# Performance work log

Hardware: AMD Instinct MI355X
Metric: run time of the kernel (lower is better)

## Reference

```python
import jax, jax.numpy as jnp
import numpy as np

B, T, E, D = 4, 1024, 1024, 2048   # batch, dec len, enc len, model dim
N, K, H = 16, 8, 256               # q heads, kv heads, head dim
G = N // K                         # GQA group size
SCALE = H ** -0.5                  # query_pre_attn_scalar
SOFT_CAP = 50.0
EPS = 1e-6
ROPE_BASE = 10000.0
_K_MASK = jnp.finfo(jnp.bfloat16).min


def _rms_norm(x, scale, eps=EPS):
    var = jnp.mean(jnp.square(x), axis=-1, keepdims=True)
    return x * jax.lax.rsqrt(var + eps) * (1.0 + scale)


def _apply_rope(x, positions, base=ROPE_BASE):
    # x: [B, L, n, H], positions: [B, L]; rope_proportion=1.0, scale_factor=1.0
    h = x.shape[-1]
    freq_exp = 2.0 / h * jnp.arange(h // 2, dtype=jnp.float32)
    timescale = base ** freq_exp                                  # [H/2]
    ang = (positions.astype(jnp.float32)[..., None] / timescale)[..., None, :]  # [B,L,1,H/2]
    sin, cos = jnp.sin(ang), jnp.cos(ang)
    x1, x2 = jnp.split(x, 2, axis=-1)
    out = jnp.concatenate([x1 * cos - x2 * sin, x2 * cos + x1 * sin], axis=-1)
    return out.astype(x.dtype)


def setup_inputs() -> dict:
    key = jax.random.key(0)
    ks = jax.random.split(key, 8)
    hidden_states = jax.random.normal(ks[0], (B, T, D), jnp.float32)
    encoder_hidden_states = jax.random.normal(ks[1], (B, E, D), jnp.float32)
    position_ids = jnp.broadcast_to(jnp.arange(T, dtype=jnp.int32)[None, :], (B, T))
    # merged mask: causal over self part, full visibility over cross part
    causal = jnp.tril(jnp.ones((T, T), jnp.bool_))
    cross = jnp.ones((T, E), jnp.bool_)
    merged_attention_mask = jnp.broadcast_to(
        jnp.concatenate([causal, cross], axis=-1)[None, None], (B, 1, T, T + E))
    w = 0.02
    q_w = jax.random.normal(ks[2], (N, D, H), jnp.float32) * w
    k_w = jax.random.normal(ks[3], (K, D, H), jnp.float32) * w
    v_w = jax.random.normal(ks[4], (K, D, H), jnp.float32) * w
    o_w = jax.random.normal(ks[5], (N, H, D), jnp.float32) * w
    q_scale = jax.random.normal(ks[6], (H,), jnp.float32) * w
    k_scale = jax.random.normal(ks[7], (H,), jnp.float32) * w
    return dict(hidden_states=hidden_states, encoder_hidden_states=encoder_hidden_states,
                position_ids=position_ids, merged_attention_mask=merged_attention_mask,
                q_w=q_w, k_w=k_w, v_w=v_w, o_w=o_w, q_scale=q_scale, k_scale=k_scale)


def reference(hidden_states, encoder_hidden_states, position_ids, merged_attention_mask,
              q_w, k_w, v_w, o_w, q_scale, k_scale):
    # QKV projections
    query = jnp.einsum('BTD,NDH->BTNH', hidden_states, q_w)
    self_key = jnp.einsum('BTD,KDH->BTKH', hidden_states, k_w)
    self_value = jnp.einsum('BTD,KDH->BTKH', hidden_states, v_w)
    # QK-RMSNorm
    query = _rms_norm(query, q_scale)
    self_key = _rms_norm(self_key, k_scale)
    # RoPE on self-attention q/k only
    query = _apply_rope(query, position_ids)
    self_key = _apply_rope(self_key, position_ids)
    # Cross K/V from encoder states (no RoPE)
    cross_key = _rms_norm(jnp.einsum('BTD,KDH->BTKH', encoder_hidden_states, k_w), k_scale)
    cross_value = jnp.einsum('BTD,KDH->BTKH', encoder_hidden_states, v_w)
    # Merge self + cross along key axis
    keys = jnp.concatenate([self_key, cross_key], axis=1)       # [B, T+E, K, H]
    values = jnp.concatenate([self_value, cross_value], axis=1)
    # Scaled GQA attention
    q = (query * SCALE).reshape(B, T, K, G, H)
    logits = jnp.einsum('BTKGH,BSKH->BKGTS', q, keys)
    # logit soft-capping
    logits = SOFT_CAP * jnp.tanh(logits / SOFT_CAP)
    mask = merged_attention_mask[:, :, None]                    # [B,1,1,T,S]
    logits = jnp.where(mask, logits, _K_MASK)
    probs = jax.nn.softmax(logits.astype(jnp.float32), axis=-1).astype(keys.dtype)
    attn = jnp.einsum('BKGTS,BSKH->BTKGH', probs, values).reshape(B, T, N, H)
    return jnp.einsum('BTNH,NHD->BTD', attn, o_w)
```

## Files before the change

### kernel.cpp

```cpp
#include <hip/hip_runtime.h>
#include <hip/hip_bf16.h>
#include <cstdio>


typedef __attribute__((ext_vector_type(8))) short bf16x8;
typedef __attribute__((ext_vector_type(4))) float f32x4;

static __device__ __forceinline__ ushort f2bf(float x){
  uint u = __float_as_uint(x);
  u += 0x7fffu + ((u >> 16) & 1u);
  return (ushort)(u >> 16);
}
static __device__ __forceinline__ float bf2f(ushort u){
  return __uint_as_float((uint)u << 16);
}
#define GLL16(gp, lp)                                                          \
  __builtin_amdgcn_global_load_lds(                                            \
      (const __attribute__((address_space(1))) void*)(gp),                     \
      (__attribute__((address_space(3))) void*)(lp), 16, 0, 0)

__global__ void k_detect(const uint* __restrict__ src, int* __restrict__ flag){
  int lane = threadIdx.x & 63;
  int cnt = 0;
  for (int i = 0; i < 4; i++){
    uint w = src[lane * 4 + i];
    uint e = (w >> 7) & 0xffu;
    cnt += (e >= 90u && e <= 141u) ? 1 : 0;
  }
  for (int o = 1; o < 64; o <<= 1) cnt += __shfl_xor(cnt, o);
  if (lane == 0) *flag = (cnt >= 128) ? 1 : 0;
}

__global__ void k_tobf(const void* __restrict__ src, ushort* __restrict__ dst,
                       int n8, const int* __restrict__ flag){
  int i = blockIdx.x * blockDim.x + threadIdx.x;
  if (i >= n8) return;
  if (*flag){
    reinterpret_cast<uint4*>(dst)[i] = reinterpret_cast<const uint4*>(src)[i];
  } else {
    const float4* s = reinterpret_cast<const float4*>(src);
    float4 a = s[i * 2], b = s[i * 2 + 1];
    ushort o[8] = { f2bf(a.x), f2bf(a.y), f2bf(a.z), f2bf(a.w),
                    f2bf(b.x), f2bf(b.y), f2bf(b.z), f2bf(b.w) };
    reinterpret_cast<uint4*>(dst)[i] = *reinterpret_cast<uint4*>(o);
  }
}

__global__ void k_wtrans(const void* __restrict__ in, ushort* __restrict__ out,
                         int R, int C, const int* __restrict__ flag){
  __shared__ ushort t[32][33];
  int isbf = *flag;
  int p = blockIdx.z;
  int r0 = blockIdx.y * 32, c0 = blockIdx.x * 32;
  ushort* op = out + (size_t)p * R * C;
  int cc = threadIdx.x & 31, rr = threadIdx.x >> 5;
  if (isbf){
    const ushort* ip = (const ushort*)in + (size_t)p * R * C;
    for (int i = 0; i < 32; i += 8)
      t[rr + i][cc] = ip[(size_t)(r0 + rr + i) * C + c0 + cc];
  } else {
    const float* ip = (const float*)in + (size_t)p * R * C;
    for (int i = 0; i < 32; i += 8)
      t[rr + i][cc] = f2bf(ip[(size_t)(r0 + rr + i) * C + c0 + cc]);
  }
  __syncthreads();
  for (int i = 0; i < 32; i += 8)
    op[(size_t)(c0 + rr + i) * R + r0 + cc] = t[cc][rr + i];
}

__global__ __launch_bounds__(256)
void k_gemm_qkv(const ushort* __restrict__ A0, const ushort* __restrict__ A1,
                const ushort* __restrict__ Bm,
                ushort* __restrict__ Qo, ushort* __restrict__ Ko,
                ushort* __restrict__ Vo){
  const int m0 = blockIdx.y * 128, n0 = blockIdx.x * 128;
  if (n0 < 4096 && m0 >= 4096) return;
  __shared__ ushort As[128 * 32];
  __shared__ ushort Bs[128 * 32];
  const int tid = threadIdx.x;
  const int Kd = 2048;
  const ushort* Ap = (m0 < 4096) ? (A0 + (size_t)m0 * Kd)
                                 : (A1 + (size_t)(m0 - 4096) * Kd);
  const ushort* Bp = Bm + (size_t)n0 * Kd;
  const int w = tid >> 6, lane = tid & 63, c = lane & 15, q = lane >> 4;
  const int wr = (w >> 1) * 64, wc = (w & 1) * 64;

  f32x4 zf = {0.f, 0.f, 0.f, 0.f};
  f32x4 acc[4][4];
  for (int mi = 0; mi < 4; mi++) for (int ni = 0; ni < 4; ni++) acc[mi][ni] = zf;

  const int sr = tid >> 2, sc8 = (tid & 3) * 8;
  const ushort* ga = Ap + (size_t)sr * Kd + sc8;
  const ushort* gb = Bp + (size_t)sr * Kd + sc8;
  ushort* la = &As[sr * 32 + sc8];
  ushort* lb = &Bs[sr * 32 + sc8];
  const size_t rowskip = (size_t)64 * Kd;

  for (int k0 = 0; k0 < Kd; k0 += 32){
    GLL16(ga + k0,           la);
    GLL16(ga + k0 + rowskip, la + 64 * 32);
    GLL16(gb + k0,           lb);
    GLL16(gb + k0 + rowskip, lb + 64 * 32);
    __syncthreads();
    bf16x8 af[4], bfrg[4];
    for (int mi = 0; mi < 4; mi++)
      af[mi] = *reinterpret_cast<const bf16x8*>(&As[(wr + mi * 16 + c) * 32 + q * 8]);
    for (int ni = 0; ni < 4; ni++)
      bfrg[ni] = *reinterpret_cast<const bf16x8*>(&Bs[(wc + ni * 16 + c) * 32 + q * 8]);
    for (int mi = 0; mi < 4; mi++)
      for (int ni = 0; ni < 4; ni++)
        acc[mi][ni] = __builtin_amdgcn_mfma_f32_16x16x32_bf16(af[mi], bfrg[ni], acc[mi][ni], 0, 0, 0);
    __syncthreads();
  }

  for (int mi = 0; mi < 4; mi++)
    for (int ni = 0; ni < 4; ni++){
      int gr0 = m0 + wr + mi * 16 + q * 4;
      int gc  = n0 + wc + ni * 16 + c;
      if (n0 < 4096){
        for (int r = 0; r < 4; r++)
          Qo[(size_t)(gr0 + r) * 4096 + gc] = f2bf(acc[mi][ni][r]);
      } else if (n0 < 6144){
        int col = gc - 4096;
        for (int r = 0; r < 4; r++){
          int gr = gr0 + r, b, s;
          if (gr < 4096){ b = gr >> 10; s = gr & 1023; }
          else { int g2 = gr - 4096; b = g2 >> 10; s = 1024 + (g2 & 1023); }
          Ko[(size_t)(b * 2048 + s) * 2048 + col] = f2bf(acc[mi][ni][r]);
        }
      } else {
        int col = gc - 6144;
        int gr = gr0, b, s;
        if (gr < 4096){ b = gr >> 10; s = gr & 1023; }
        else { int g2 = gr - 4096; b = g2 >> 10; s = 1024 + (g2 & 1023); }
        int kk = col >> 8, h = col & 255;
        ushort4 o;
        o.x = f2bf(acc[mi][ni][0]); o.y = f2bf(acc[mi][ni][1]);
        o.z = f2bf(acc[mi][ni][2]); o.w = f2bf(acc[mi][ni][3]);
        *reinterpret_cast<ushort4*>(Vo + ((size_t)(b * 8 + kk) * 256 + h) * 2048 + s) = o;
      }
    }
}

__global__ __launch_bounds__(256)
void k_gemm_o(const ushort* __restrict__ A0, const ushort* __restrict__ Bm,
              float* __restrict__ Cout, int N, int Kd){
  __shared__ ushort As[128 * 32];
  __shared__ ushort Bs[128 * 32];
  const int tid = threadIdx.x;
  const int m0 = blockIdx.y * 128, n0 = blockIdx.x * 128;
  const ushort* Ap = A0 + (size_t)m0 * Kd;
  const ushort* Bp = Bm + (size_t)n0 * Kd;
  const int w = tid >> 6, lane = tid & 63, c = lane & 15, q = lane >> 4;
  const int wr = (w >> 1) * 64, wc = (w & 1) * 64;
  f32x4 zf = {0.f, 0.f, 0.f, 0.f};
  f32x4 acc[4][4];
  for (int mi = 0; mi < 4; mi++) for (int ni = 0; ni < 4; ni++) acc[mi][ni] = zf;
  const int sr = tid >> 2, sc8 = (tid & 3) * 8;
  const ushort* ga = Ap + (size_t)sr * Kd + sc8;
  const ushort* gb = Bp + (size_t)sr * Kd + sc8;
  ushort* la = &As[sr * 32 + sc8];
  ushort* lb = &Bs[sr * 32 + sc8];
  const size_t rowskip = (size_t)64 * Kd;
  for (int k0 = 0; k0 < Kd; k0 += 32){
    GLL16(ga + k0,           la);
    GLL16(ga + k0 + rowskip, la + 64 * 32);
    GLL16(gb + k0,           lb);
    GLL16(gb + k0 + rowskip, lb + 64 * 32);
    __syncthreads();
    bf16x8 af[4], bfrg[4];
    for (int mi = 0; mi < 4; mi++)
      af[mi] = *reinterpret_cast<const bf16x8*>(&As[(wr + mi * 16 + c) * 32 + q * 8]);
    for (int ni = 0; ni < 4; ni++)
      bfrg[ni] = *reinterpret_cast<const bf16x8*>(&Bs[(wc + ni * 16 + c) * 32 + q * 8]);
    for (int mi = 0; mi < 4; mi++)
      for (int ni = 0; ni < 4; ni++)
        acc[mi][ni] = __builtin_amdgcn_mfma_f32_16x16x32_bf16(af[mi], bfrg[ni], acc[mi][ni], 0, 0, 0);
    __syncthreads();
  }
  for (int mi = 0; mi < 4; mi++)
    for (int ni = 0; ni < 4; ni++){
      int gr0 = m0 + wr + mi * 16 + q * 4;
      int gc  = n0 + wc + ni * 16 + c;
      for (int r = 0; r < 4; r++)
        Cout[(size_t)(gr0 + r) * N + gc] = acc[mi][ni][r];
    }
}

__global__ __launch_bounds__(256)
void k_norm_q(const ushort* __restrict__ Qraw, const int* __restrict__ pos,
              const ushort* __restrict__ scale, ushort* __restrict__ Qbf){
  int w = threadIdx.x >> 6, lane = threadIdx.x & 63;
  int gw = blockIdx.x * 4 + w;
  int bt = gw >> 4;
  ushort4 xu = *reinterpret_cast<const ushort4*>(Qraw + (size_t)gw * 256 + lane * 4);
  float x[4] = { bf2f(xu.x), bf2f(xu.y), bf2f(xu.z), bf2f(xu.w) };
  float ss = x[0]*x[0] + x[1]*x[1] + x[2]*x[2] + x[3]*x[3];
  for (int o = 32; o > 0; o >>= 1) ss += __shfl_xor(ss, o);
  float rin = rsqrtf(ss * (1.f / 256.f) + 1e-6f);
  ushort4 su = *reinterpret_cast<const ushort4*>(scale + lane * 4);
  float y[4] = { x[0] * rin * (1.f + bf2f(su.x)), x[1] * rin * (1.f + bf2f(su.y)),
                 x[2] * rin * (1.f + bf2f(su.z)), x[3] * rin * (1.f + bf2f(su.w)) };
  float oth[4];
  for (int i = 0; i < 4; i++) oth[i] = __shfl_xor(y[i], 32);
  bool hi = lane >= 32;
  float fb = (float)((lane & 31) * 4);
  float p = (float)pos[bt];
  ushort4 o;
  ushort* op[4] = {&o.x, &o.y, &o.z, &o.w};
  for (int i = 0; i < 4; i++){
    float fi = fb + i;
    float tsi = expf(fi * -0.07195578415f);
    float ang = p * tsi;
    float sn, cs; sincosf(ang, &sn, &cs);
    float v = hi ? (y[i] * cs + oth[i] * sn) : (y[i] * cs - oth[i] * sn);
    *op[i] = f2bf(v * 0.0625f);
  }
  *reinterpret_cast<ushort4*>(Qbf + (size_t)gw * 256 + lane * 4) = o;
}

__global__ __launch_bounds__(256)
void k_norm_k(const ushort* __restrict__ Kraw, const int* __restrict__ pos,
              const ushort* __restrict__ scale, ushort* __restrict__ Kbf){
  int w = threadIdx.x >> 6, lane = threadIdx.x & 63;
  int gw = blockIdx.x * 4 + w;
  int row = gw >> 3;
  int s = row & 2047, b = row >> 11;
  ushort4 xu = *reinterpret_cast<const ushort4*>(Kraw + (size_t)gw * 256 + lane * 4);
  float x[4] = { bf2f(xu.x), bf2f(xu.y), bf2f(xu.z), bf2f(xu.w) };
  float ss = x[0]*x[0] + x[1]*x[1] + x[2]*x[2] + x[3]*x[3];
  for (int o = 32; o > 0; o >>= 1) ss += __shfl_xor(ss, o);
  float rin = rsqrtf(ss * (1.f / 256.f) + 1e-6f);
  ushort4 su = *reinterpret_cast<const ushort4*>(scale + lane * 4);
  float y[4] = { x[0] * rin * (1.f + bf2f(su.x)), x[1] * rin * (1.f + bf2f(su.y)),
                 x[2] * rin * (1.f + bf2f(su.z)), x[3] * rin * (1.f + bf2f(su.w)) };
  ushort4 o;
  ushort* op[4] = {&o.x, &o.y, &o.z, &o.w};
  if (s < 1024){
    float oth[4];
    for (int i = 0; i < 4; i++) oth[i] = __shfl_xor(y[i], 32);
    bool hi = lane >= 32;
    float fb = (float)((lane & 31) * 4);
    float p = (float)pos[b * 1024 + s];
    for (int i = 0; i < 4; i++){
      float fi = fb + i;
      float tsi = expf(fi * -0.07195578415f);
      float ang = p * tsi;
      float sn, cs; sincosf(ang, &sn, &cs);
      float v = hi ? (y[i] * cs + oth[i] * sn) : (y[i] * cs - oth[i] * sn);
      *op[i] = f2bf(v);
    }
  } else {
    for (int i = 0; i < 4; i++) *op[i] = f2bf(y[i]);
  }
  *reinterpret_cast<ushort4*>(Kbf + (size_t)gw * 256 + lane * 4) = o;
}

__global__ __launch_bounds__(256)
void k_attn(const ushort* __restrict__ Qbf, const ushort* __restrict__ Kbf,
            const ushort* __restrict__ Vt, ushort* __restrict__ attn){
  constexpr int PSs = 40;
  __shared__ ushort Ks2[2][32 * 256];
  __shared__ ushort Vs2[2][256 * 32];
  __shared__ ushort Pm[4][32 * PSs];
  int id = blockIdx.x;
  int xcd = id & 7, slot = id >> 3;
  int gl  = slot >> 4;
  int grp = xcd + 8 * gl;
  int w16 = slot & 15;
  int b = grp >> 3, kk = grp & 7;
  int a16 = w16 >> 1, p16 = w16 & 1;
  int hh = a16 & 1, xx = a16 >> 1;
  int j0 = p16 ? 7 - xx : xx;
  int j  = (gl >= 2) ? 7 - j0 : j0;
  int n = kk * 2 + hh;
  int t0 = j * 128;
  int tid = threadIdx.x, w = tid >> 6, lane = tid & 63, c = lane & 15, q = lane >> 4;
  int rowbase = t0 + w * 32;

  bf16x8 qf[2][8];
  for (int g = 0; g < 2; g++){
    int tq = rowbase + g * 16 + c;
    const ushort* qp = Qbf + ((size_t)(b * 1024 + tq) * 16 + n) * 256 + q * 8;
    for (int f = 0; f < 8; f++) qf[g][f] = *reinterpret_cast<const bf16x8*>(qp + f * 32);
  }
  f32x4 zf = {0.f, 0.f, 0.f, 0.f};
  f32x4 accO[2][16];
  for (int g = 0; g < 2; g++) for (int i = 0; i < 16; i++) accO[g][i] = zf;
  float lacc[2][4] = {{0.f,0.f,0.f,0.f},{0.f,0.f,0.f,0.f}};

  const ushort* Kbase = Kbf + ((size_t)b * 2048 * 8 + kk) * 256;
  const ushort* Vbase = Vt + (size_t)(b * 8 + kk) * 256 * 2048;
  int nself = (t0 >> 5) + 4;
  int ntile = nself + 32;

#define STAGE(bf, s0v)                                                         \
  do {                                                                         \
    const ushort* kp_ = Kbase + (size_t)(s0v) * 2048;                          \
    const ushort* vp_ = Vbase + (s0v);                                         \
    _Pragma("unroll")                                                          \
    for (int i_ = 0; i_ < 4; i_++){                                            \
      int tau_ = tid + i_ * 256;                                               \
      int r_ = tau_ >> 5, kch_ = tau_ & 31;                                    \
      GLL16(kp_ + r_ * 2048 + ((kch_ ^ (r_ & 7)) << 3), &Ks2[bf][tau_ * 8]);   \
    }                                                                          \
    _Pragma("unroll")                                                          \
    for (int i_ = 0; i_ < 4; i_++){                                            \
      int tau_ = tid + i_ * 256;                                               \
      int h_ = tau_ >> 2, k2_ = tau_ & 3;                                      \
      GLL16(vp_ + h_ * 2048 + (k2_ << 3), &Vs2[bf][tau_ * 8]);                 \
    }                                                                          \
  } while (0)

  STAGE(0, 0);
  int cur = 0;
  const int cxor = c & 7;

  for (int it = 0; it < ntile; ++it){
    int s0 = (it < nself) ? it * 32 : 1024 + (it - nself) * 32;
    __builtin_amdgcn_sched_barrier(0);
    __builtin_amdgcn_s_barrier();
    __builtin_amdgcn_sched_barrier(0);
    if (it + 1 < ntile){
      int itn = it + 1;
      int s0n = (itn < nself) ? itn * 32 : 1024 + (itn - nself) * 32;
      STAGE(cur ^ 1, s0n);
      __asm__ volatile("s_waitcnt vmcnt(8)" ::: "memory");
    } else {
      __asm__ volatile("s_waitcnt vmcnt(0)" ::: "memory");
    }
    __builtin_amdgcn_sched_barrier(0);
    __builtin_amdgcn_s_barrier();
    __builtin_amdgcn_sched_barrier(0);

    const ushort* Kcur = Ks2[cur];
    const ushort* Vcur = Vs2[cur];
    f32x4 accL[2][2];
    accL[0][0] = zf; accL[0][1] = zf; accL[1][0] = zf; accL[1][1] = zf;
    for (int ni = 0; ni < 2; ni++)
      for (int f = 0; f < 8; f++){
        bf16x8 kb = *reinterpret_cast<const bf16x8*>(
            &Kcur[(ni * 16 + c) * 256 + (((f * 4 + q) ^ cxor) << 3)]);
        accL[0][ni] = __builtin_amdgcn_mfma_f32_16x16x32_bf16(qf[0][f], kb, accL[0][ni], 0, 0, 0);
        accL[1][ni] = __builtin_amdgcn_mfma_f32_16x16x32_bf16(qf[1][f], kb, accL[1][ni], 0, 0, 0);
      }
    ushort* pw = Pm[w];
    for (int g = 0; g < 2; g++)
      for (int ni = 0; ni < 2; ni++)
        for (int r = 0; r < 4; r++){
          int s = s0 + ni * 16 + c;
          int t = rowbase + g * 16 + q * 4 + r;
          float e2 = __expf(accL[g][ni][r] * 0.04f);
          float d = __builtin_amdgcn_rcpf(e2 + 1.f);
          float pv = (s >= 1024 || s <= t)
                       ? 5.184705529e21f * __expf(-100.f * d) : 0.f;
          lacc[g][r] += pv;
          pw[(g * 16 + q * 4 + r) * PSs + ni * 16 + c] = f2bf(pv);
        }
    __asm__ volatile("s_waitcnt lgkmcnt(0)" ::: "memory");
    bf16x8 pa0 = *reinterpret_cast<const bf16x8*>(&pw[c * PSs + q * 8]);
    bf16x8 pa1 = *reinterpret_cast<const bf16x8*>(&pw[(16 + c) * PSs + q * 8]);
    for (int hi = 0; hi < 16; hi++){
      bf16x8 vb = *reinterpret_cast<const bf16x8*>(&Vcur[(hi * 16 + c) * 32 + q * 8]);
      accO[0][hi] = __builtin_amdgcn_mfma_f32_16x16x32_bf16(pa0, vb, accO[0][hi], 0, 0, 0);
      accO[1][hi] = __builtin_amdgcn_mfma_f32_16x16x32_bf16(pa1, vb, accO[1][hi], 0, 0, 0);
    }
    __builtin_amdgcn_sched_barrier(0);
    cur ^= 1;
  }
#undef STAGE
  for (int g = 0; g < 2; g++)
    for (int r = 0; r < 4; r++)
      for (int o = 1; o < 16; o <<= 1) lacc[g][r] += __shfl_xor(lacc[g][r], o);
  for (int g = 0; g < 2; g++){
    float inv[4];
    for (int r = 0; r < 4; r++) inv[r] = 1.f / fmaxf(lacc[g][r], 1e-37f);
    for (int hi = 0; hi < 16; hi++)
      for (int r = 0; r < 4; r++){
        int t = rowbase + g * 16 + q * 4 + r;
        attn[((size_t)(b * 1024 + t) * 16 + n) * 256 + hi * 16 + c] = f2bf(accO[g][hi][r] * inv[r]);
      }
  }
}

extern "C" void kernel_launch(void* const* d_in, const int* in_sizes, int n_in,
                              void* d_out, int out_size, void* d_ws, size_t ws_size,
                              hipStream_t stream){
  const void* hidden = d_in[0];
  const void* enc    = d_in[1];
  const int*  posids = (const int*)d_in[2];
  const void* qw = d_in[4];
  const void* kw = d_in[5];
  const void* vw = d_in[6];
  const void* ow = d_in[7];
  const void* qs = d_in[8];
  const void* ks = d_in[9];
  float* out = (float*)d_out;

  char* ws = (char*)d_ws;
  size_t off = 0;
  auto alloc = [&](size_t sz){ void* p = ws + off; off += sz; return p; };
  char*   HbEb = (char*)alloc(33554432);
  ushort* Hb   = (ushort*)HbEb;
  ushort* Eb   = (ushort*)(HbEb + 16777216);
  ushort* Wcat = (ushort*)alloc(33554432);
  ushort* Wo   = (ushort*)alloc(16777216);
  ushort* Qraw = (ushort*)alloc(33554432);
  ushort* Kraw = (ushort*)alloc(33554432);
  ushort* Vt   = (ushort*)alloc(33554432);
  ushort* qsb  = (ushort*)alloc(512);
  ushort* ksb  = (ushort*)alloc(512);
  int*    flag = (int*)alloc(64);
  ushort* Qbf   = (ushort*)HbEb;
  ushort* Kbf   = Qraw;
  ushort* attnb = Kraw;
  if (off > ws_size){
    fprintf(stderr, "kernel_launch: ws too small: need %zu, have %zu\n", off, ws_size);
    return;
  }

  k_detect<<<1, 64, 0, stream>>>((const uint*)hidden, flag);
  k_tobf<<<4096, 256, 0, stream>>>(hidden, Hb, 1048576, flag);
  k_tobf<<<4096, 256, 0, stream>>>(enc,    Eb, 1048576, flag);
  k_tobf<<<1, 256, 0, stream>>>(qs, qsb, 32, flag);
  k_tobf<<<1, 256, 0, stream>>>(ks, ksb, 32, flag);

  k_wtrans<<<dim3(8, 64, 16), 256, 0, stream>>>(qw, Wcat,            2048, 256, flag);
  k_wtrans<<<dim3(8, 64, 8),  256, 0, stream>>>(kw, Wcat + 8388608,  2048, 256, flag);
  k_wtrans<<<dim3(8, 64, 8),  256, 0, stream>>>(vw, Wcat + 12582912, 2048, 256, flag);
  k_wtrans<<<dim3(64, 128, 1), 256, 0, stream>>>(ow, Wo, 4096, 2048, flag);

  k_gemm_qkv<<<dim3(64, 64), 256, 0, stream>>>(Hb, Eb, Wcat, Qraw, Kraw, Vt);

  k_norm_q<<<16384, 256, 0, stream>>>(Qraw, posids, qsb, Qbf);
  k_norm_k<<<16384, 256, 0, stream>>>(Kraw, posids, ksb, Kbf);

  k_attn<<<512, 256, 0, stream>>>(Qbf, Kbf, Vt, attnb);

  k_gemm_o<<<dim3(16, 32), 256, 0, stream>>>(attnb, Wo, out, 2048, 4096);
}
```

Measured before the change: 900.8 us.

## Use atomic work queue with longest-first job order in attention kernel

The attention kernel no longer maps each block to a fixed tile. A global counter, reset in the preceding norm kernel, hands out jobs so the longest causal tiles (high j) are taken first. Blocks loop until the queue is empty, which should even out the load caused by causal imbalance. It also adds an XOR swizzle on the V shared-memory tile to reduce LDS bank conflicts. The cost is an atomic plus a barrier per job, and the previous XCD-aware tile placement is lost, which may hurt L2 locality.

Result: faster. 878.4 us (-2.5%).

```diff
diff --git a/kernel.cpp b/kernel.cpp
--- a/kernel.cpp
+++ b/kernel.cpp
@@ -221,7 +221,9 @@
 
 __global__ __launch_bounds__(256)
 void k_norm_k(const ushort* __restrict__ Kraw, const int* __restrict__ pos,
-              const ushort* __restrict__ scale, ushort* __restrict__ Kbf){
+              const ushort* __restrict__ scale, ushort* __restrict__ Kbf,
+              int* __restrict__ ctr){
+  if (blockIdx.x == 0 && threadIdx.x == 0) *ctr = 0;
   int w = threadIdx.x >> 6, lane = threadIdx.x & 63;
   int gw = blockIdx.x * 4 + w;
   int row = gw >> 3;
@@ -258,128 +260,139 @@
 
 __global__ __launch_bounds__(256)
 void k_attn(const ushort* __restrict__ Qbf, const ushort* __restrict__ Kbf,
-            const ushort* __restrict__ Vt, ushort* __restrict__ attn){
+            const ushort* __restrict__ Vt, ushort* __restrict__ attn,
+            int* __restrict__ ctr){
   constexpr int PSs = 40;
   __shared__ ushort Ks2[2][32 * 256];
   __shared__ ushort Vs2[2][256 * 32];
   __shared__ ushort Pm[4][32 * PSs];
-  int id = blockIdx.x;
-  int xcd = id & 7, slot = id >> 3;
-  int gl  = slot >> 4;
-  int grp = xcd + 8 * gl;
-  int w16 = slot & 15;
-  int b = grp >> 3, kk = grp & 7;
-  int a16 = w16 >> 1, p16 = w16 & 1;
-  int hh = a16 & 1, xx = a16 >> 1;
-  int j0 = p16 ? 7 - xx : xx;
-  int j  = (gl >= 2) ? 7 - j0 : j0;
-  int n = kk * 2 + hh;
-  int t0 = j * 128;
+  __shared__ int jobS;
+
   int tid = threadIdx.x, w = tid >> 6, lane = tid & 63, c = lane & 15, q = lane >> 4;
-  int rowbase = t0 + w * 32;
-
-  bf16x8 qf[2][8];
-  for (int g = 0; g < 2; g++){
-    int tq = rowbase + g * 16 + c;
-    const ushort* qp = Qbf + ((size_t)(b * 1024 + tq) * 16 + n) * 256 + q * 8;
-    for (int f = 0; f < 8; f++) qf[g][f] = *reinterpret_cast<const bf16x8*>(qp + f * 32);
-  }
+  const int cxor = c & 7;
+  const int vxor = (c >> 1) & 3;
+  int cur = 0;
   f32x4 zf = {0.f, 0.f, 0.f, 0.f};
-  f32x4 accO[2][16];
-  for (int g = 0; g < 2; g++) for (int i = 0; i < 16; i++) accO[g][i] = zf;
-  float lacc[2][4] = {{0.f,0.f,0.f,0.f},{0.f,0.f,0.f,0.f}};
-
-  const ushort* Kbase = Kbf + ((size_t)b * 2048 * 8 + kk) * 256;
-  const ushort* Vbase = Vt + (size_t)(b * 8 + kk) * 256 * 2048;
-  int nself = (t0 >> 5) + 4;
-  int ntile = nself + 32;
+
+  int ktau[4], vtau[4];
+#pragma unroll
+  for (int i = 0; i < 4; i++){ ktau[i] = tid + i * 256; vtau[i] = tid + i * 256; }
+
+  for (;;){
+    if (tid == 0) jobS = atomicAdd(ctr, 1);
+    __syncthreads();
+    int job = jobS;
+    if (job >= 512) return;
+    int grp = job & 31;
+    int within = job >> 5;
+    int b = grp >> 3, kk = grp & 7;
+    int n = kk * 2 + (within & 1);
+    int j = 7 - (within >> 1);
+    int t0 = j * 128;
+    int rowbase = t0 + w * 32;
+
+    const ushort* Kbase = Kbf + ((size_t)b * 2048 * 8 + kk) * 256;
+    const ushort* Vbase = Vt + (size_t)(b * 8 + kk) * 256 * 2048;
+    int nself = (t0 >> 5) + 4;
+    int ntile = nself + 32;
+
+    bf16x8 qf[2][8];
+    for (int g = 0; g < 2; g++){
+      int tq = rowbase + g * 16 + c;
+      const ushort* qp = Qbf + ((size_t)(b * 1024 + tq) * 16 + n) * 256 + q * 8;
+      for (int f = 0; f < 8; f++) qf[g][f] = *reinterpret_cast<const bf16x8*>(qp + f * 32);
+    }
+    f32x4 accO[2][16];
+    for (int g = 0; g < 2; g++) for (int i = 0; i < 16; i++) accO[g][i] = zf;
+    float lacc[2][4] = {{0.f,0.f,0.f,0.f},{0.f,0.f,0.f,0.f}};
 
 #define STAGE(bf, s0v)                                                         \
-  do {                                                                         \
-    const ushort* kp_ = Kbase + (size_t)(s0v) * 2048;                          \
-    const ushort* vp_ = Vbase + (s0v);                                         \
-    _Pragma("unroll")                                                          \
-    for (int i_ = 0; i_ < 4; i_++){                                            \
-      int tau_ = tid + i_ * 256;                                               \
-      int r_ = tau_ >> 5, kch_ = tau_ & 31;                                    \
-      GLL16(kp_ + r_ * 2048 + ((kch_ ^ (r_ & 7)) << 3), &Ks2[bf][tau_ * 8]);   \
-    }                                                                          \
-    _Pragma("unroll")                                                          \
-    for (int i_ = 0; i_ < 4; i_++){                                            \
-      int tau_ = tid + i_ * 256;                                               \
-      int h_ = tau_ >> 2, k2_ = tau_ & 3;                                      \
-      GLL16(vp_ + h_ * 2048 + (k2_ << 3), &Vs2[bf][tau_ * 8]);                 \
-    }                                                                          \
-  } while (0)
-
-  STAGE(0, 0);
-  int cur = 0;
-  const int cxor = c & 7;
-
-  for (int it = 0; it < ntile; ++it){
-    int s0 = (it < nself) ? it * 32 : 1024 + (it - nself) * 32;
-    __builtin_amdgcn_sched_barrier(0);
-    __builtin_amdgcn_s_barrier();
-    __builtin_amdgcn_sched_barrier(0);
-    if (it + 1 < ntile){
-      int itn = it + 1;
-      int s0n = (itn < nself) ? itn * 32 : 1024 + (itn - nself) * 32;
-      STAGE(cur ^ 1, s0n);
-      __asm__ volatile("s_waitcnt vmcnt(8)" ::: "memory");
-    } else {
-      __asm__ volatile("s_waitcnt vmcnt(0)" ::: "memory");
-    }
-    __builtin_amdgcn_sched_barrier(0);
-    __builtin_amdgcn_s_barrier();
-    __builtin_amdgcn_sched_barrier(0);
-
-    const ushort* Kcur = Ks2[cur];
-    const ushort* Vcur = Vs2[cur];
-    f32x4 accL[2][2];
-    accL[0][0] = zf; accL[0][1] = zf; accL[1][0] = zf; accL[1][1] = zf;
-    for (int ni = 0; ni < 2; ni++)
-      for (int f = 0; f < 8; f++){
-        bf16x8 kb = *reinterpret_cast<const bf16x8*>(
-            &Kcur[(ni * 16 + c) * 256 + (((f * 4 + q) ^ cxor) << 3)]);
-        accL[0][ni] = __builtin_amdgcn_mfma_f32_16x16x32_bf16(qf[0][f], kb, accL[0][ni], 0, 0, 0);
-        accL[1][ni] = __builtin_amdgcn_mfma_f32_16x16x32_bf16(qf[1][f], kb, accL[1][ni], 0, 0, 0);
+    do {                                                                       \
+      const ushort* kp_ = Kbase + (size_t)(s0v) * 2048;                        \
+      const ushort* vp_ = Vbase + (s0v);                                       \
+      _Pragma("unroll")                                                        \
+      for (int i_ = 0; i_ < 4; i_++){                                          \
+        int tau_ = ktau[i_];                                                   \
+        int r_ = tau_ >> 5, kch_ = tau_ & 31;                                  \
+        GLL16(kp_ + r_ * 2048 + ((kch_ ^ (r_ & 7)) << 3), &Ks2[bf][tau_ * 8]); \
+      }                                                                        \
+      _Pragma("unroll")                                                        \
+      for (int i_ = 0; i_ < 4; i_++){                                          \
+        int tau_ = vtau[i_];                                                   \
+        int h_ = tau_ >> 2, k2_ = tau_ & 3;                                    \
+        GLL16(vp_ + h_ * 2048 + ((k2_ ^ ((h_ >> 1) & 3)) << 3),                \
+              &Vs2[bf][tau_ * 8]);                                             \
+      }                                                                        \
+    } while (0)
+
+    STAGE(cur, 0);
+
+    for (int it = 0; it < ntile; ++it){
+      int s0 = (it < nself) ? it * 32 : 1024 + (it - nself) * 32;
+      __builtin_amdgcn_sched_barrier(0);
+      __builtin_amdgcn_s_barrier();
+      __builtin_amdgcn_sched_barrier(0);
+      if (it + 1 < ntile){
+        int itn = it + 1;
+        int s0n = (itn < nself) ? itn * 32 : 1024 + (itn - nself) * 32;
+        STAGE(cur ^ 1, s0n);
+        __asm__ volatile("s_waitcnt vmcnt(8)" ::: "memory");
+      } else {
+        __asm__ volatile("s_waitcnt vmcnt(0)" ::: "memory");
       }
-    ushort* pw = Pm[w];
+      __builtin_amdgcn_sched_barrier(0);
+      __builtin_amdgcn_s_barrier();
+      __builtin_amdgcn_sched_barrier(0);
+
+      const ushort* Kcur = Ks2[cur];
+      const ushort* Vcur = Vs2[cur];
+      f32x4 accL[2][2];
+      accL[0][0] = zf; accL[0][1] = zf; accL[1][0] = zf; accL[1][1] = zf;
+      for (int ni = 0; ni < 2; ni++)
+        for (int f = 0; f < 8; f++){
+          bf16x8 kb = *reinterpret_cast<const bf16x8*>(
+              &Kcur[(ni * 16 + c) * 256 + (((f * 4 + q) ^ cxor) << 3)]);
+          accL[0][ni] = __builtin_amdgcn_mfma_f32_16x16x32_bf16(qf[0][f], kb, accL[0][ni], 0, 0, 0);
+          accL[1][ni] = __builtin_amdgcn_mfma_f32_16x16x32_bf16(qf[1][f], kb, accL[1][ni], 0, 0, 0);
+        }
+      ushort* pw = Pm[w];
+      for (int g = 0; g < 2; g++)
+        for (int ni = 0; ni < 2; ni++)
+          for (int r = 0; r < 4; r++){
+            int s = s0 + ni * 16 + c;
+            int t = rowbase + g * 16 + q * 4 + r;
+            float e2 = __expf(accL[g][ni][r] * 0.04f);
+            float d = __builtin_amdgcn_rcpf(e2 + 1.f);
+            float pv = (s >= 1024 || s <= t)
+                         ? 5.184705529e21f * __expf(-100.f * d) : 0.f;
+            lacc[g][r] += pv;
+            pw[(g * 16 + q * 4 + r) * PSs + ni * 16 + c] = f2bf(pv);
+          }
+      __asm__ volatile("s_waitcnt lgkmcnt(0)" ::: "memory");
+      bf16x8 pa0 = *reinterpret_cast<const bf16x8*>(&pw[c * PSs + q * 8]);
+      bf16x8 pa1 = *reinterpret_cast<const bf16x8*>(&pw[(16 + c) * PSs + q * 8]);
+      for (int hi = 0; hi < 16; hi++){
+        bf16x8 vb = *reinterpret_cast<const bf16x8*>(
+            &Vcur[(hi * 16 + c) * 32 + ((q ^ vxor) << 3)]);
+        accO[0][hi] = __builtin_amdgcn_mfma_f32_16x16x32_bf16(pa0, vb, accO[0][hi], 0, 0, 0);
+        accO[1][hi] = __builtin_amdgcn_mfma_f32_16x16x32_bf16(pa1, vb, accO[1][hi], 0, 0, 0);
+      }
+      __builtin_amdgcn_sched_barrier(0);
+      cur ^= 1;
+    }
+#undef STAGE
     for (int g = 0; g < 2; g++)
-      for (int ni = 0; ni < 2; ni++)
+      for (int r = 0; r < 4; r++)
+        for (int o = 1; o < 16; o <<= 1) lacc[g][r] += __shfl_xor(lacc[g][r], o);
+    for (int g = 0; g < 2; g++){
+      float inv[4];
+      for (int r = 0; r < 4; r++) inv[r] = 1.f / fmaxf(lacc[g][r], 1e-37f);
+      for (int hi = 0; hi < 16; hi++)
         for (int r = 0; r < 4; r++){
-          int s = s0 + ni * 16 + c;
           int t = rowbase + g * 16 + q * 4 + r;
-          float e2 = __expf(accL[g][ni][r] * 0.04f);
-          float d = __builtin_amdgcn_rcpf(e2 + 1.f);
-          float pv = (s >= 1024 || s <= t)
-                       ? 5.184705529e21f * __expf(-100.f * d) : 0.f;
-          lacc[g][r] += pv;
-          pw[(g * 16 + q * 4 + r) * PSs + ni * 16 + c] = f2bf(pv);
+          attn[((size_t)(b * 1024 + t) * 16 + n) * 256 + hi * 16 + c] = f2bf(accO[g][hi][r] * inv[r]);
         }
-    __asm__ volatile("s_waitcnt lgkmcnt(0)" ::: "memory");
-    bf16x8 pa0 = *reinterpret_cast<const bf16x8*>(&pw[c * PSs + q * 8]);
-    bf16x8 pa1 = *reinterpret_cast<const bf16x8*>(&pw[(16 + c) * PSs + q * 8]);
-    for (int hi = 0; hi < 16; hi++){
-      bf16x8 vb = *reinterpret_cast<const bf16x8*>(&Vcur[(hi * 16 + c) * 32 + q * 8]);
-      accO[0][hi] = __builtin_amdgcn_mfma_f32_16x16x32_bf16(pa0, vb, accO[0][hi], 0, 0, 0);
-      accO[1][hi] = __builtin_amdgcn_mfma_f32_16x16x32_bf16(pa1, vb, accO[1][hi], 0, 0, 0);
-    }
-    __builtin_amdgcn_sched_barrier(0);
-    cur ^= 1;
-  }
-#undef STAGE
-  for (int g = 0; g < 2; g++)
-    for (int r = 0; r < 4; r++)
-      for (int o = 1; o < 16; o <<= 1) lacc[g][r] += __shfl_xor(lacc[g][r], o);
-  for (int g = 0; g < 2; g++){
-    float inv[4];
-    for (int r = 0; r < 4; r++) inv[r] = 1.f / fmaxf(lacc[g][r], 1e-37f);
-    for (int hi = 0; hi < 16; hi++)
-      for (int r = 0; r < 4; r++){
-        int t = rowbase + g * 16 + q * 4 + r;
-        attn[((size_t)(b * 1024 + t) * 16 + n) * 256 + hi * 16 + c] = f2bf(accO[g][hi][r] * inv[r]);
-      }
+    }
   }
 }
 
@@ -411,6 +424,7 @@
   ushort* qsb  = (ushort*)alloc(512);
   ushort* ksb  = (ushort*)alloc(512);
   int*    flag = (int*)alloc(64);
+  int*    ctr  = flag + 4;
   ushort* Qbf   = (ushort*)HbEb;
   ushort* Kbf   = Qraw;
   ushort* attnb = Kraw;
@@ -433,9 +447,9 @@
   k_gemm_qkv<<<dim3(64, 64), 256, 0, stream>>>(Hb, Eb, Wcat, Qraw, Kraw, Vt);
 
   k_norm_q<<<16384, 256, 0, stream>>>(Qraw, posids, qsb, Qbf);
-  k_norm_k<<<16384, 256, 0, stream>>>(Kraw, posids, ksb, Kbf);
-
-  k_attn<<<512, 256, 0, stream>>>(Qbf, Kbf, Vt, attnb);
+  k_norm_k<<<16384, 256, 0, stream>>>(Kraw, posids, ksb, Kbf, ctr);
+
+  k_attn<<<512, 256, 0, stream>>>(Qbf, Kbf, Vt, attnb, ctr);
 
   k_gemm_o<<<dim3(16, 32), 256, 0, stream>>>(attnb, Wo, out, 2048, 4096);
 }
```
